# Optimization experiments

Measured on AMD Instinct MI355X. Metric: run time of the kernel, lower is better.

Reference implementation:

```python
import jax, jax.numpy as jnp
import numpy as np

HID = 128
IN = 28
SEQ = 28
NUM_LAYERS = 10  # num_classes mistakenly passed as num_layers in the source
NUM_CLASSES = 10


def setup_inputs() -> dict:
    key = jax.random.key(0)
    ks = jax.random.split(key, 9)
    s = 1.0 / np.sqrt(HID)  # pytorch nn.RNN init scale
    x = jax.random.normal(ks[0], (4096, SEQ, IN), dtype=jnp.float32)
    W_ih0 = jax.random.uniform(ks[1], (HID, IN), jnp.float32, -s, s)
    W_ih = jax.random.uniform(ks[2], (NUM_LAYERS - 1, HID, HID), jnp.float32, -s, s)
    W_hh = jax.random.uniform(ks[3], (NUM_LAYERS, HID, HID), jnp.float32, -s, s)
    b_ih = jax.random.uniform(ks[4], (NUM_LAYERS, HID), jnp.float32, -s, s)
    b_hh = jax.random.uniform(ks[5], (NUM_LAYERS, HID), jnp.float32, -s, s)
    fc_W = jax.random.uniform(ks[6], (NUM_CLASSES, HID), jnp.float32, -s, s)
    fc_b = jax.random.uniform(ks[7], (NUM_CLASSES,), jnp.float32, -s, s)
    return {"x": x, "W_ih0": W_ih0, "W_ih": W_ih, "W_hh": W_hh,
            "b_ih": b_ih, "b_hh": b_hh, "fc_W": fc_W, "fc_b": fc_b}


def _rnn_layer(xs, Wih, Whh, bih, bhh):
    # xs: [B, T, F]; precompute the input projection once (batched GEMM),
    # then scan only the recurrent matmul + tanh.
    B = xs.shape[0]
    xp = jnp.einsum('btf,hf->bth', xs, Wih) + bih + bhh  # [B, T, H]

    def step(h, xp_t):
        h = jnp.tanh(xp_t + h @ Whh.T)
        return h, h

    h0 = jnp.zeros((B, Whh.shape[0]), xs.dtype)
    _, ys = jax.lax.scan(step, h0, jnp.swapaxes(xp, 0, 1))  # [T, B, H]
    return jnp.swapaxes(ys, 0, 1)  # [B, T, H]


def reference(x, W_ih0, W_ih, W_hh, b_ih, b_hh, fc_W, fc_b):
    x = x.reshape(-1, SEQ, IN)
    h = _rnn_layer(x, W_ih0, W_hh[0], b_ih[0], b_hh[0])
    for l in range(1, NUM_LAYERS):
        h = _rnn_layer(h, W_ih[l - 1], W_hh[l], b_ih[l], b_hh[l])
    # fc on last timestep
    return h[:, -1, :] @ fc_W.T + fc_b
```

## Files before the change

kernel.cpp:

```cpp
#include <hip/hip_runtime.h>
#include <cstdint>
#include <cstddef>

#define HID 128
#define SEQL 28
#define INP 28
#define NL 10
#define NC 10
#define BATCH 4096
#define BB 16
#define STRD 136
#define BUFH (16 * STRD)

#define NSLOT 37
#define LDS_BYTES (NSLOT * BUFH * 2)

typedef _Float16 half8 __attribute__((ext_vector_type(8)));
typedef _Float16 half4 __attribute__((ext_vector_type(4)));
typedef float    f32x4 __attribute__((ext_vector_type(4)));

#define WS_WCAT_OFF 0
#define WS_BIAS_OFF 655360

__global__ void convert_weights(const float* __restrict__ Wih0,
                                const float* __restrict__ Wih,
                                const float* __restrict__ Whh,
                                const float* __restrict__ bih,
                                const float* __restrict__ bhh,
                                _Float16* __restrict__ Wcat,
                                float* __restrict__ bias) {
  int tg = blockIdx.x * blockDim.x + threadIdx.x;
  if (tg >= NL * HID * 16) return;
  int r = tg >> 4, seg = tg & 15;
  int l = r / HID, n = r % HID;
  int k0 = seg * 16;
  _Float16* dst = Wcat + (size_t)r * 256 + k0;
  if (l == 0) {
#pragma unroll
    for (int i = 0; i < 16; ++i) {
      int k = k0 + i;
      float v = 0.f;
      if (k < INP) v = Wih0[n * INP + k];
      else if (k >= HID) v = Whh[(size_t)n * HID + (k - HID)];
      dst[i] = (_Float16)v;
    }
  } else {
    const float* src = (k0 < HID)
        ? (Wih + ((size_t)(l - 1) * HID + n) * HID + k0)
        : (Whh + ((size_t)l * HID + n) * HID + (k0 - HID));
#pragma unroll
    for (int i = 0; i < 16; ++i) dst[i] = (_Float16)src[i];
  }
  if (seg == 0) bias[r] = bih[r] + bhh[r];
}

__device__ __forceinline__ float tanh_fast(float v) {
  float e = __builtin_amdgcn_exp2f(v * 2.8853900817779268f);
  float r = __builtin_amdgcn_rcpf(e + 1.f);
  return __builtin_fmaf(-2.f, r, 1.f);
}

__device__ __forceinline__ void barrier_light() {
  __builtin_amdgcn_sched_barrier(0);
  asm volatile("s_waitcnt lgkmcnt(0)" ::: "memory");
  __builtin_amdgcn_s_barrier();
  __builtin_amdgcn_sched_barrier(0);
}

__global__ __launch_bounds__(512, 2) void rnn_fused(
    const float* __restrict__ x,
    const _Float16* __restrict__ Wcat,
    const float* __restrict__ bias,
    const float* __restrict__ fcW,
    const float* __restrict__ fcb,
    float* __restrict__ out) {
  extern __shared__ __align__(16) _Float16 lds[];

  const int tid    = threadIdx.x;
  const int lane15 = tid & 15;
  const int quad   = (tid >> 4) & 3;
  const int wid    = tid >> 6;
  const int s      = wid >> 1;
  const int nhalf  = wid & 1;
  const int n0     = nhalf * 64;
  const int b0     = blockIdx.x * BB;
  const int frow0  = tid >> 3;
  const int fc0    = (tid & 7) * 4;

  const int rdoff = lane15 * STRD + quad * 8;
  const int wroff = lane15 * STRD + n0 + quad * 4;

  half8 wf[4][8];
  f32x4 bias4[4];

  for (int g = 0; g < 3; ++g) {
    const int L = g * 4 + s;
    if (L < NL) {
      const _Float16* Wl = Wcat + (size_t)L * HID * 256;
#pragma unroll
      for (int nn = 0; nn < 4; ++nn) {
#pragma unroll
        for (int ks = 0; ks < 8; ++ks)
          wf[nn][ks] = *(const half8*)(Wl + (size_t)(n0 + nn * 16 + lane15) * 256 + ks * 32 + quad * 8);
        bias4[nn] = *(const f32x4*)(bias + L * HID + n0 + nn * 16 + quad * 4);
      }
    }
    __syncthreads();
    {
      uint4 z; z.x = z.y = z.z = z.w = 0u;
      for (int i = tid; i < (BUFH * 7) / 8; i += 512)
        ((uint4*)(lds + 2 * BUFH))[i] = z;
    }

    f32x4 pfx[2];

    auto load_next = [&](int t, int sl) {
      if (tid < 128) {
        const float* xb = x + ((size_t)(b0 + frow0) * SEQL + t) * INP;
        if (fc0 < INP) pfx[sl] = *(const f32x4*)(xb + fc0);
        else { f32x4 z4 = {0.f, 0.f, 0.f, 0.f}; pfx[sl] = z4; }
      }
    };
    auto store_X = [&](int sl) {
      if (tid < 128) {
        _Float16 h4[4];
#pragma unroll
        for (int i = 0; i < 4; ++i) h4[i] = (_Float16)pfx[sl][i];
        *(uint2*)(lds + sl * BUFH + frow0 * STRD + fc0) = *(const uint2*)h4;
      }
    };

    if (g == 0) {
      load_next(0, 0);
      store_X(0);
      load_next(1, 1);
    }

    auto tick = [&](int tau, int pt) {
      barrier_light();
      if (g == 0 && tau + 2 < SEQL) load_next(tau + 2, pt);
      const int t = tau - s;
      if (L < NL && (unsigned)t < SEQL) {
        const _Float16* INb;
        if (s == 0) INb = (g == 0) ? lds + pt * BUFH : lds + (9 + t) * BUFH;
        else        INb = lds + (2 + 2 * (s - 1) + (1 - pt)) * BUFH;
        const _Float16* Hb = (s == 3)
            ? ((t == 0) ? lds + 8 * BUFH : lds + (9 + (t - 1)) * BUFH)
            : lds + (2 + 2 * s + (1 - pt)) * BUFH;
        _Float16* Ob = (s == 3) ? lds + (9 + t) * BUFH
                                : lds + (2 + 2 * s + pt) * BUFH;

        auto tw = [&](int nn, f32x4 av) {
          half4 o;
#pragma unroll
          for (int r = 0; r < 4; ++r) o[r] = (_Float16)tanh_fast(av[r]);
          *(half4*)(Ob + wroff + nn * 16) = o;
        };

        if (g == 0 && s == 0) {
          half8 ax = *(const half8*)(INb + rdoff);
          half8 ah[4];
#pragma unroll
          for (int ks = 0; ks < 4; ++ks) ah[ks] = *(const half8*)(Hb + rdoff + ks * 32);
          f32x4 a0 = bias4[0], a1 = bias4[1];
          a0 = __builtin_amdgcn_mfma_f32_16x16x32_f16(wf[0][0], ax, a0, 0, 0, 0);
          a1 = __builtin_amdgcn_mfma_f32_16x16x32_f16(wf[1][0], ax, a1, 0, 0, 0);
#pragma unroll
          for (int ks = 0; ks < 4; ++ks) {
            a0 = __builtin_amdgcn_mfma_f32_16x16x32_f16(wf[0][4 + ks], ah[ks], a0, 0, 0, 0);
            a1 = __builtin_amdgcn_mfma_f32_16x16x32_f16(wf[1][4 + ks], ah[ks], a1, 0, 0, 0);
          }
          f32x4 a2 = bias4[2], a3 = bias4[3];
          a2 = __builtin_amdgcn_mfma_f32_16x16x32_f16(wf[2][0], ax, a2, 0, 0, 0);
          a3 = __builtin_amdgcn_mfma_f32_16x16x32_f16(wf[3][0], ax, a3, 0, 0, 0);
#pragma unroll
          for (int ks = 0; ks < 4; ++ks) {
            a2 = __builtin_amdgcn_mfma_f32_16x16x32_f16(wf[2][4 + ks], ah[ks], a2, 0, 0, 0);
            a3 = __builtin_amdgcn_mfma_f32_16x16x32_f16(wf[3][4 + ks], ah[ks], a3, 0, 0, 0);
          }
          tw(0, a0); tw(1, a1); tw(2, a2); tw(3, a3);
        } else {
          half8 af[8];
#pragma unroll
          for (int ks = 0; ks < 4; ++ks) af[ks] = *(const half8*)(INb + rdoff + ks * 32);
#pragma unroll
          for (int ks = 0; ks < 4; ++ks) af[4 + ks] = *(const half8*)(Hb + rdoff + ks * 32);
          f32x4 a0 = bias4[0], a1 = bias4[1];
#pragma unroll
          for (int i = 0; i < 8; ++i) {
            a0 = __builtin_amdgcn_mfma_f32_16x16x32_f16(wf[0][i], af[i], a0, 0, 0, 0);
            a1 = __builtin_amdgcn_mfma_f32_16x16x32_f16(wf[1][i], af[i], a1, 0, 0, 0);
          }
          f32x4 a2 = bias4[2], a3 = bias4[3];
#pragma unroll
          for (int i = 0; i < 8; ++i) {
            a2 = __builtin_amdgcn_mfma_f32_16x16x32_f16(wf[2][i], af[i], a2, 0, 0, 0);
            a3 = __builtin_amdgcn_mfma_f32_16x16x32_f16(wf[3][i], af[i], a3, 0, 0, 0);
          }
          tw(0, a0); tw(1, a1); tw(2, a2); tw(3, a3);
        }
      }
      if (g == 0 && tau + 1 < SEQL) store_X(1 - pt);
    };

    const int Tend = (g == 2) ? 28 : 30;
    for (int tau = 0; tau < Tend; tau += 2) {
      tick(tau, 0);
      tick(tau + 1, 1);
    }
    tick(Tend, 0);
  }
  __syncthreads();

  if (tid < BB * NC) {
    int c = tid >> 4;
    int b = tid & 15;
    float acc = fcb[c];
    const float* wr = fcW + c * HID;
    const _Float16* hr = lds + BUFH * 4 + b * STRD;
#pragma unroll
    for (int k0 = 0; k0 < HID; k0 += 8) {
      half8 h = *(const half8*)(hr + k0);
      f32x4 w0 = *(const f32x4*)(wr + k0);
      f32x4 w1 = *(const f32x4*)(wr + k0 + 4);
#pragma unroll
      for (int j = 0; j < 4; ++j)
        acc += (float)h[j] * w0[j] + (float)h[j + 4] * w1[j];
    }
    out[(size_t)(b0 + b) * NC + c] = acc;
  }
}

extern "C" void kernel_launch(void* const* d_in, const int* in_sizes, int n_in,
                              void* d_out, int out_size, void* d_ws, size_t ws_size,
                              hipStream_t stream) {
  const float* x    = (const float*)d_in[0];
  const float* Wih0 = (const float*)d_in[1];
  const float* Wih  = (const float*)d_in[2];
  const float* Whh  = (const float*)d_in[3];
  const float* bih  = (const float*)d_in[4];
  const float* bhh  = (const float*)d_in[5];
  const float* fcW  = (const float*)d_in[6];
  const float* fcb  = (const float*)d_in[7];
  float* out = (float*)d_out;

  _Float16* Wcat = (_Float16*)((char*)d_ws + WS_WCAT_OFF);
  float*    bs   = (float*)((char*)d_ws + WS_BIAS_OFF);

  static bool attr_done = false;
  if (!attr_done) {
    hipFuncSetAttribute(reinterpret_cast<const void*>(rnn_fused),
                        hipFuncAttributeMaxDynamicSharedMemorySize, LDS_BYTES);
    attr_done = true;
  }

  convert_weights<<<dim3(80), dim3(256), 0, stream>>>(Wih0, Wih, Whh, bih, bhh, Wcat, bs);
  rnn_fused<<<dim3(BATCH / BB), dim3(512), LDS_BYTES, stream>>>(x, Wcat, bs, fcW, fcb, out);
}
```

Measured before the change: 180.5 us.

## Load layer-0 input directly into MFMA registers and skip zero-state work

Layer-0 input x is now loaded by the computing waves straight into half8 MFMA operand registers, prefetched one step ahead, instead of being staged through LDS slots by 128 threads. At t=0 the hidden-state MFMAs and LDS reads are skipped rather than multiplying a zeroed buffer, which also removes the per-group zeroing of LDS. The LDS slot layout is compacted from 37 to 34 buffers. The cost is that each wave does its own global load of x one tick ahead, so its latency is only partly hidden, plus extra register pressure from axbuf.

```diff
diff --git a/kernel.cpp b/kernel.cpp
--- a/kernel.cpp
+++ b/kernel.cpp
@@ -12,7 +12,7 @@
 #define STRD 136
 #define BUFH (16 * STRD)
 
-#define NSLOT 37
+#define NSLOT 34
 #define LDS_BYTES (NSLOT * BUFH * 2)
 
 typedef _Float16 half8 __attribute__((ext_vector_type(8)));
@@ -81,17 +81,26 @@
   const int quad   = (tid >> 4) & 3;
   const int wid    = tid >> 6;
   const int s      = wid >> 1;
-  const int nhalf  = wid & 1;
-  const int n0     = nhalf * 64;
+  const int n0     = (wid & 1) * 64;
   const int b0     = blockIdx.x * BB;
-  const int frow0  = tid >> 3;
-  const int fc0    = (tid & 7) * 4;
 
   const int rdoff = lane15 * STRD + quad * 8;
   const int wroff = lane15 * STRD + n0 + quad * 4;
 
   half8 wf[4][8];
   f32x4 bias4[4];
+  half8 axbuf[2];
+
+  auto load_x = [&](int t, int sl) {
+    const float* xr = x + ((size_t)(b0 + lane15) * SEQL + t) * INP;
+    f32x4 xa = *(const f32x4*)(xr + quad * 8);
+    f32x4 xb = {0.f, 0.f, 0.f, 0.f};
+    if (quad < 3) xb = *(const f32x4*)(xr + quad * 8 + 4);
+    half8 ax;
+#pragma unroll
+    for (int i = 0; i < 4; ++i) { ax[i] = (_Float16)xa[i]; ax[4 + i] = (_Float16)xb[i]; }
+    axbuf[sl] = ax;
+  };
 
   for (int g = 0; g < 3; ++g) {
     const int L = g * 4 + s;
@@ -106,50 +115,14 @@
       }
     }
     __syncthreads();
-    {
-      uint4 z; z.x = z.y = z.z = z.w = 0u;
-      for (int i = tid; i < (BUFH * 7) / 8; i += 512)
-        ((uint4*)(lds + 2 * BUFH))[i] = z;
-    }
-
-    f32x4 pfx[2];
-
-    auto load_next = [&](int t, int sl) {
-      if (tid < 128) {
-        const float* xb = x + ((size_t)(b0 + frow0) * SEQL + t) * INP;
-        if (fc0 < INP) pfx[sl] = *(const f32x4*)(xb + fc0);
-        else { f32x4 z4 = {0.f, 0.f, 0.f, 0.f}; pfx[sl] = z4; }
-      }
-    };
-    auto store_X = [&](int sl) {
-      if (tid < 128) {
-        _Float16 h4[4];
-#pragma unroll
-        for (int i = 0; i < 4; ++i) h4[i] = (_Float16)pfx[sl][i];
-        *(uint2*)(lds + sl * BUFH + frow0 * STRD + fc0) = *(const uint2*)h4;
-      }
-    };
-
-    if (g == 0) {
-      load_next(0, 0);
-      store_X(0);
-      load_next(1, 1);
-    }
+    if (g == 0 && s == 0) load_x(0, 0);
 
     auto tick = [&](int tau, int pt) {
       barrier_light();
-      if (g == 0 && tau + 2 < SEQL) load_next(tau + 2, pt);
       const int t = tau - s;
       if (L < NL && (unsigned)t < SEQL) {
-        const _Float16* INb;
-        if (s == 0) INb = (g == 0) ? lds + pt * BUFH : lds + (9 + t) * BUFH;
-        else        INb = lds + (2 + 2 * (s - 1) + (1 - pt)) * BUFH;
-        const _Float16* Hb = (s == 3)
-            ? ((t == 0) ? lds + 8 * BUFH : lds + (9 + (t - 1)) * BUFH)
-            : lds + (2 + 2 * s + (1 - pt)) * BUFH;
-        _Float16* Ob = (s == 3) ? lds + (9 + t) * BUFH
-                                : lds + (2 + 2 * s + pt) * BUFH;
-
+        _Float16* Ob = (s == 3) ? lds + (size_t)(6 + t) * BUFH
+                                : lds + (size_t)(2 * s + pt) * BUFH;
         auto tw = [&](int nn, f32x4 av) {
           half4 o;
 #pragma unroll
@@ -158,49 +131,79 @@
         };
 
         if (g == 0 && s == 0) {
-          half8 ax = *(const half8*)(INb + rdoff);
-          half8 ah[4];
-#pragma unroll
-          for (int ks = 0; ks < 4; ++ks) ah[ks] = *(const half8*)(Hb + rdoff + ks * 32);
-          f32x4 a0 = bias4[0], a1 = bias4[1];
-          a0 = __builtin_amdgcn_mfma_f32_16x16x32_f16(wf[0][0], ax, a0, 0, 0, 0);
-          a1 = __builtin_amdgcn_mfma_f32_16x16x32_f16(wf[1][0], ax, a1, 0, 0, 0);
-#pragma unroll
-          for (int ks = 0; ks < 4; ++ks) {
-            a0 = __builtin_amdgcn_mfma_f32_16x16x32_f16(wf[0][4 + ks], ah[ks], a0, 0, 0, 0);
-            a1 = __builtin_amdgcn_mfma_f32_16x16x32_f16(wf[1][4 + ks], ah[ks], a1, 0, 0, 0);
+          half8 ax = axbuf[pt];
+          if (t > 0) {
+            const _Float16* Hb = lds + (size_t)(1 - pt) * BUFH;
+            half8 ah[4];
+#pragma unroll
+            for (int ks = 0; ks < 4; ++ks) ah[ks] = *(const half8*)(Hb + rdoff + ks * 32);
+            f32x4 a0 = bias4[0], a1 = bias4[1];
+            a0 = __builtin_amdgcn_mfma_f32_16x16x32_f16(wf[0][0], ax, a0, 0, 0, 0);
+            a1 = __builtin_amdgcn_mfma_f32_16x16x32_f16(wf[1][0], ax, a1, 0, 0, 0);
+#pragma unroll
+            for (int ks = 0; ks < 4; ++ks) {
+              a0 = __builtin_amdgcn_mfma_f32_16x16x32_f16(wf[0][4 + ks], ah[ks], a0, 0, 0, 0);
+              a1 = __builtin_amdgcn_mfma_f32_16x16x32_f16(wf[1][4 + ks], ah[ks], a1, 0, 0, 0);
+            }
+            f32x4 a2 = bias4[2], a3 = bias4[3];
+            a2 = __builtin_amdgcn_mfma_f32_16x16x32_f16(wf[2][0], ax, a2, 0, 0, 0);
+            a3 = __builtin_amdgcn_mfma_f32_16x16x32_f16(wf[3][0], ax, a3, 0, 0, 0);
+#pragma unroll
+            for (int ks = 0; ks < 4; ++ks) {
+              a2 = __builtin_amdgcn_mfma_f32_16x16x32_f16(wf[2][4 + ks], ah[ks], a2, 0, 0, 0);
+              a3 = __builtin_amdgcn_mfma_f32_16x16x32_f16(wf[3][4 + ks], ah[ks], a3, 0, 0, 0);
+            }
+            tw(0, a0); tw(1, a1); tw(2, a2); tw(3, a3);
+          } else {
+            f32x4 a0 = bias4[0], a1 = bias4[1], a2 = bias4[2], a3 = bias4[3];
+            a0 = __builtin_amdgcn_mfma_f32_16x16x32_f16(wf[0][0], ax, a0, 0, 0, 0);
+            a1 = __builtin_amdgcn_mfma_f32_16x16x32_f16(wf[1][0], ax, a1, 0, 0, 0);
+            a2 = __builtin_amdgcn_mfma_f32_16x16x32_f16(wf[2][0], ax, a2, 0, 0, 0);
+            a3 = __builtin_amdgcn_mfma_f32_16x16x32_f16(wf[3][0], ax, a3, 0, 0, 0);
+            tw(0, a0); tw(1, a1); tw(2, a2); tw(3, a3);
           }
-          f32x4 a2 = bias4[2], a3 = bias4[3];
-          a2 = __builtin_amdgcn_mfma_f32_16x16x32_f16(wf[2][0], ax, a2, 0, 0, 0);
-          a3 = __builtin_amdgcn_mfma_f32_16x16x32_f16(wf[3][0], ax, a3, 0, 0, 0);
-#pragma unroll
-          for (int ks = 0; ks < 4; ++ks) {
-            a2 = __builtin_amdgcn_mfma_f32_16x16x32_f16(wf[2][4 + ks], ah[ks], a2, 0, 0, 0);
-            a3 = __builtin_amdgcn_mfma_f32_16x16x32_f16(wf[3][4 + ks], ah[ks], a3, 0, 0, 0);
+        } else {
+          const _Float16* INb = (s == 0) ? lds + (size_t)(6 + t) * BUFH
+                                         : lds + (size_t)(2 * (s - 1) + (1 - pt)) * BUFH;
+          half8 af[8];
+#pragma unroll
+          for (int ks = 0; ks < 4; ++ks) af[ks] = *(const half8*)(INb + rdoff + ks * 32);
+          if (t > 0) {
+            const _Float16* Hb = (s == 3) ? lds + (size_t)(6 + (t - 1)) * BUFH
+                                          : lds + (size_t)(2 * s + (1 - pt)) * BUFH;
+#pragma unroll
+            for (int ks = 0; ks < 4; ++ks) af[4 + ks] = *(const half8*)(Hb + rdoff + ks * 32);
+            f32x4 a0 = bias4[0], a1 = bias4[1];
+#pragma unroll
+            for (int i = 0; i < 8; ++i) {
+              a0 = __builtin_amdgcn_mfma_f32_16x16x32_f16(wf[0][i], af[i], a0, 0, 0, 0);
+              a1 = __builtin_amdgcn_mfma_f32_16x16x32_f16(wf[1][i], af[i], a1, 0, 0, 0);
+            }
+            f32x4 a2 = bias4[2], a3 = bias4[3];
+#pragma unroll
+            for (int i = 0; i < 8; ++i) {
+              a2 = __builtin_amdgcn_mfma_f32_16x16x32_f16(wf[2][i], af[i], a2, 0, 0, 0);
+              a3 = __builtin_amdgcn_mfma_f32_16x16x32_f16(wf[3][i], af[i], a3, 0, 0, 0);
+            }
+            tw(0, a0); tw(1, a1); tw(2, a2); tw(3, a3);
+          } else {
+            f32x4 a0 = bias4[0], a1 = bias4[1];
+#pragma unroll
+            for (int i = 0; i < 4; ++i) {
+              a0 = __builtin_amdgcn_mfma_f32_16x16x32_f16(wf[0][i], af[i], a0, 0, 0, 0);
+              a1 = __builtin_amdgcn_mfma_f32_16x16x32_f16(wf[1][i], af[i], a1, 0, 0, 0);
+            }
+            f32x4 a2 = bias4[2], a3 = bias4[3];
+#pragma unroll
+            for (int i = 0; i < 4; ++i) {
+              a2 = __builtin_amdgcn_mfma_f32_16x16x32_f16(wf[2][i], af[i], a2, 0, 0, 0);
+              a3 = __builtin_amdgcn_mfma_f32_16x16x32_f16(wf[3][i], af[i], a3, 0, 0, 0);
+            }
+            tw(0, a0); tw(1, a1); tw(2, a2); tw(3, a3);
           }
-          tw(0, a0); tw(1, a1); tw(2, a2); tw(3, a3);
-        } else {
-          half8 af[8];
-#pragma unroll
-          for (int ks = 0; ks < 4; ++ks) af[ks] = *(const half8*)(INb + rdoff + ks * 32);
-#pragma unroll
-          for (int ks = 0; ks < 4; ++ks) af[4 + ks] = *(const half8*)(Hb + rdoff + ks * 32);
-          f32x4 a0 = bias4[0], a1 = bias4[1];
-#pragma unroll
-          for (int i = 0; i < 8; ++i) {
-            a0 = __builtin_amdgcn_mfma_f32_16x16x32_f16(wf[0][i], af[i], a0, 0, 0, 0);
-            a1 = __builtin_amdgcn_mfma_f32_16x16x32_f16(wf[1][i], af[i], a1, 0, 0, 0);
-          }
-          f32x4 a2 = bias4[2], a3 = bias4[3];
-#pragma unroll
-          for (int i = 0; i < 8; ++i) {
-            a2 = __builtin_amdgcn_mfma_f32_16x16x32_f16(wf[2][i], af[i], a2, 0, 0, 0);
-            a3 = __builtin_amdgcn_mfma_f32_16x16x32_f16(wf[3][i], af[i], a3, 0, 0, 0);
-          }
-          tw(0, a0); tw(1, a1); tw(2, a2); tw(3, a3);
         }
       }
-      if (g == 0 && tau + 1 < SEQL) store_X(1 - pt);
+      if (g == 0 && s == 0 && tau + 1 < SEQL) load_x(tau + 1, 1 - pt);
     };
 
     const int Tend = (g == 2) ? 28 : 30;
@@ -217,7 +220,7 @@
     int b = tid & 15;
     float acc = fcb[c];
     const float* wr = fcW + c * HID;
-    const _Float16* hr = lds + BUFH * 4 + b * STRD;
+    const _Float16* hr = lds + 2 * BUFH + b * STRD;
 #pragma unroll
     for (int k0 = 0; k0 < HID; k0 += 8) {
       half8 h = *(const half8*)(hr + k0);
```

Measured after the change: 178.3 us. Within noise of the previous version (-1.2%).
